# Kernel tuning notes

Hardware: AMD Instinct MI355X
Metric: run time of the kernel (lower is better)

## Reference

```python
import jax, jax.numpy as jnp
import numpy as np

NUM_HEADS = 16
D_ATT = 64


def setup_inputs() -> dict:
    key = jax.random.key(0)
    ks = jax.random.split(key, 7)
    b, n, hd = 4, 2048, NUM_HEADS * 64  # input last dim = num_heads * per-head embed_dim
    Q_vec = jax.random.normal(ks[0], (b, n, hd), dtype=jnp.float32)
    K_vec = jax.random.normal(ks[1], (b, n, hd), dtype=jnp.float32)
    V_vec = jax.random.normal(ks[2], (b, n, hd), dtype=jnp.float32)
    # torch Linear weights: [out_features, in_features] = [d_attention, per_head_dim]
    W_Q = jax.random.normal(ks[3], (D_ATT, 64), dtype=jnp.float32) * 0.02
    W_K = jax.random.normal(ks[4], (D_ATT, 64), dtype=jnp.float32) * 0.02
    W_V = jax.random.normal(ks[5], (D_ATT, 64), dtype=jnp.float32) * 0.02
    mask = jax.random.bernoulli(ks[6], p=0.9, shape=(b, n))  # bool [b, n]
    return {"Q_vec": Q_vec, "K_vec": K_vec, "V_vec": V_vec,
            "W_Q": W_Q, "W_K": W_K, "W_V": W_V, "mask": mask}


def reference(Q_vec, K_vec, V_vec, W_Q, W_K, W_V, mask):
    b, n, _ = Q_vec.shape
    h = NUM_HEADS
    scaling = 1.0 / np.sqrt(D_ATT).astype(np.float32)

    def split_heads(x):  # b n (h d) -> b h n d
        return x.reshape(b, n, h, -1).transpose(0, 2, 1, 3)

    # Linear applied per-head (weights are [out, in]; y = x @ W^T)
    q = split_heads(Q_vec) @ W_Q.T  # [b,h,n,D_ATT]
    k = split_heads(K_vec) @ W_K.T
    v = split_heads(V_vec) @ W_V.T

    dots = jnp.einsum('bhid,bhjd->bhij', q, k) * scaling  # [b,h,n,n]
    pair_mask = mask[:, None, :] & mask[:, :, None]       # [b,n,n]
    mask_value = -jnp.finfo(dots.dtype).max
    dots = jnp.where(pair_mask[:, None, :, :], dots, mask_value)
    attn = jax.nn.softmax(dots, axis=-1)
    out = jnp.einsum('bhij,bhjd->bhid', attn, v)          # [b,h,n,D_ATT]
    return out.transpose(0, 2, 1, 3).reshape(b, n, h * D_ATT)
```

## Files before the change

### kernel.cpp

```cpp
#include <hip/hip_runtime.h>

#define B_  4
#define N_  2048
#define H_  16
#define HD_ 1024

typedef short  bf16x8 __attribute__((ext_vector_type(8)));
typedef short  bf16x4 __attribute__((ext_vector_type(4)));
typedef float  f32x4  __attribute__((ext_vector_type(4)));

static __device__ __forceinline__ unsigned short f2bf(float f) {
    unsigned int u = __builtin_bit_cast(unsigned int, f);
    u += 0x7FFFu + ((u >> 16) & 1u);
    return (unsigned short)(u >> 16);
}

static __device__ __forceinline__ unsigned rne_hi(float f) {
    unsigned u = __builtin_bit_cast(unsigned, f);
    return u + 0x7FFFu + ((u >> 16) & 1u);
}
static __device__ __forceinline__ unsigned f2bf2pack(float lo, float hi) {
    return __builtin_amdgcn_perm(rne_hi(hi), rne_hi(lo), 0x07060302u);
}

__global__ __launch_bounds__(256) void proj_kernel(
    const float* __restrict__ Qv, const float* __restrict__ Kv,
    const float* __restrict__ Vv, const float* __restrict__ WQ,
    const float* __restrict__ WK, const float* __restrict__ WV,
    unsigned short* __restrict__ qs, unsigned short* __restrict__ ks,
    unsigned short* __restrict__ vt)
{
    __shared__ __align__(16) unsigned short xb[64][72];
    __shared__ __align__(16) unsigned short Wb[64][72];
    unsigned short (*sb)[72] = xb;

    const int tid  = threadIdx.x;
    const int wq   = tid >> 6;
    const int lane = tid & 63;
    const int l15  = lane & 15;
    const int quad = lane >> 4;

    const int i0 = blockIdx.x * 64;
    const int h  = blockIdx.y;
    const int bz = blockIdx.z;
    const int b  = bz / 3;
    const int p  = bz - b * 3;

    const size_t inbase = ((size_t)b * N_ + i0) * HD_ + h * 64;
    const size_t bh     = (size_t)b * H_ + h;

    const float* W   = (p == 0) ? WQ : (p == 1) ? WK : WV;
    const float* inp = ((p == 0) ? Qv : (p == 1) ? Kv : Vv) + inbase;

    for (int v = tid; v < 1024; v += 256) {
        int tok = v >> 4, c4 = (v & 15) * 4;
        float4 f = *reinterpret_cast<const float4*>(inp + (size_t)tok * HD_ + c4);
        uint2 u;
        u.x = f2bf2pack(f.x, f.y);
        u.y = f2bf2pack(f.z, f.w);
        *reinterpret_cast<uint2*>(&xb[tok][c4]) = u;
        float4 g = *reinterpret_cast<const float4*>(W + (size_t)v * 4);
        uint2 w2;
        w2.x = f2bf2pack(g.x, g.y);
        w2.y = f2bf2pack(g.z, g.w);
        *reinterpret_cast<uint2*>(&Wb[tok][c4]) = w2;
    }
    __syncthreads();

    bf16x8 ax[2];
    #pragma unroll
    for (int kh = 0; kh < 2; ++kh)
        ax[kh] = *reinterpret_cast<const bf16x8*>(&xb[wq * 16 + l15][kh * 32 + quad * 8]);

    f32x4 C[4];
    #pragma unroll
    for (int t = 0; t < 4; ++t) {
        C[t] = f32x4{0.f, 0.f, 0.f, 0.f};
        #pragma unroll
        for (int kh = 0; kh < 2; ++kh) {
            bf16x8 bw = *reinterpret_cast<const bf16x8*>(&Wb[t * 16 + l15][kh * 32 + quad * 8]);
            C[t] = __builtin_amdgcn_mfma_f32_16x16x32_bf16(ax[kh], bw, C[t], 0, 0, 0);
        }
    }

    __syncthreads();

    if (p < 2) {
        const float scl = (p == 0) ? 0.180336880f : 1.f;
        #pragma unroll
        for (int t = 0; t < 4; ++t)
            #pragma unroll
            for (int r = 0; r < 4; ++r)
                sb[wq * 16 + quad * 4 + r][t * 16 + l15] = f2bf(C[t][r] * scl);
        __syncthreads();
        unsigned short* dst = ((p == 0) ? qs : ks) + ((size_t)bh * N_ + i0) * 64;
        for (int v = tid; v < 512; v += 256) {
            int row = v >> 3, c0 = (v & 7) * 8;
            *reinterpret_cast<uint4*>(dst + (size_t)row * 64 + c0) =
                *reinterpret_cast<const uint4*>(&sb[row][c0]);
        }
    } else {
        #pragma unroll
        for (int t = 0; t < 4; ++t) {
            uint2 u;
            u.x = f2bf2pack(C[t][0], C[t][1]);
            u.y = f2bf2pack(C[t][2], C[t][3]);
            *reinterpret_cast<uint2*>(&sb[t * 16 + l15][wq * 16 + quad * 4]) = u;
        }
        __syncthreads();
        unsigned short* vdst = vt + (size_t)bh * 64 * N_ + i0;
        for (int v = tid; v < 512; v += 256) {
            int d = v >> 3, c0 = (v & 7) * 8;
            *reinterpret_cast<uint4*>(vdst + (size_t)d * N_ + c0) =
                *reinterpret_cast<const uint4*>(&sb[d][c0]);
        }
    }
}

__global__ __launch_bounds__(256, 2) void attn_kernel(
    const unsigned short* __restrict__ qs, const unsigned short* __restrict__ ks,
    const unsigned short* __restrict__ vt, const int* __restrict__ maskp,
    float* __restrict__ out)
{
    __shared__ __align__(16) unsigned short Ks[64][72];
    __shared__ __align__(16) unsigned short Vt[64][68];
    __shared__ float kb[64];

    const int tid  = threadIdx.x;
    const int w    = tid >> 6;
    const int lane = tid & 63;
    const int l15  = lane & 15;
    const int quad = lane >> 4;

    const int i0 = blockIdx.x * 256;
    const int bh = blockIdx.y;
    const int b  = bh >> 4;
    const int h  = bh & 15;
    const int qrow0 = i0 + w * 64;

    bf16x8 aq[4][2];
    float  qm[4];
    #pragma unroll
    for (int rt = 0; rt < 4; ++rt) {
        const unsigned short* qrow = qs + ((size_t)bh * N_ + qrow0 + rt * 16 + l15) * 64;
        aq[rt][0] = *reinterpret_cast<const bf16x8*>(qrow + quad * 8);
        aq[rt][1] = *reinterpret_cast<const bf16x8*>(qrow + 32 + quad * 8);
        qm[rt] = maskp[b * N_ + qrow0 + rt * 16 + l15] ? 1.f : 0.f;
    }

    bf16x8 aones;
    #pragma unroll
    for (int j = 0; j < 8; ++j) aones[j] = (short)0x3F80;

    f32x4 O[4][4];
    f32x4 L[4];
    #pragma unroll
    for (int rt = 0; rt < 4; ++rt) {
        L[rt] = f32x4{0.f, 0.f, 0.f, 0.f};
        #pragma unroll
        for (int c = 0; c < 4; ++c) O[rt][c] = f32x4{0.f, 0.f, 0.f, 0.f};
    }

    const unsigned short* kbase = ks + (size_t)bh * N_ * 64;
    const unsigned short* vbase = vt + (size_t)bh * 64 * N_;

    for (int kv0 = 0; kv0 < N_; kv0 += 64) {
        __syncthreads();
        #pragma unroll
        for (int it = 0; it < 2; ++it) {
            int idx = tid + it * 256;
            int r = idx >> 3, g = idx & 7;
            *reinterpret_cast<uint4*>(&Ks[r][g * 8]) =
                *reinterpret_cast<const uint4*>(kbase + (size_t)(kv0 + r) * 64 + g * 8);
        }
        #pragma unroll
        for (int it = 0; it < 4; ++it) {
            int idx = tid + it * 256;
            int r = idx >> 4, g2 = idx & 15;
            *reinterpret_cast<uint2*>(&Vt[r][g2 * 4]) =
                *reinterpret_cast<const uint2*>(vbase + (size_t)r * N_ + kv0 + g2 * 4);
        }
        if (tid < 64) kb[tid] = maskp[b * N_ + kv0 + tid] ? 0.f : -1e30f;
        __syncthreads();

        bf16x8 ak[4][2];
        #pragma unroll
        for (int ct = 0; ct < 4; ++ct)
            #pragma unroll
            for (int kh = 0; kh < 2; ++kh)
                ak[ct][kh] = *reinterpret_cast<const bf16x8*>(&Ks[ct * 16 + l15][kh * 32 + quad * 8]);

        bf16x8 av[4][2];
        #pragma unroll
        for (int ct = 0; ct < 4; ++ct)
            #pragma unroll
            for (int kh = 0; kh < 2; ++kh) {
                bf16x4 lo = *reinterpret_cast<const bf16x4*>(&Vt[ct * 16 + l15][kh * 32 + quad * 4]);
                bf16x4 hi = *reinterpret_cast<const bf16x4*>(&Vt[ct * 16 + l15][kh * 32 + 16 + quad * 4]);
                av[ct][kh] = bf16x8{lo[0], lo[1], lo[2], lo[3], hi[0], hi[1], hi[2], hi[3]};
            }

        f32x4 kbv[4];
        #pragma unroll
        for (int ct = 0; ct < 4; ++ct)
            kbv[ct] = *reinterpret_cast<const f32x4*>(&kb[ct * 16 + quad * 4]);

        #pragma unroll
        for (int rt = 0; rt < 4; ++rt) {
            f32x4 S[4];
            #pragma unroll
            for (int ct = 0; ct < 4; ++ct) {
                S[ct] = kbv[ct];
                #pragma unroll
                for (int kh = 0; kh < 2; ++kh)
                    S[ct] = __builtin_amdgcn_mfma_f32_16x16x32_bf16(ak[ct][kh], aq[rt][kh], S[ct], 0, 0, 0);
            }
            unsigned pk[4][2];
            #pragma unroll
            for (int ct = 0; ct < 4; ++ct) {
                float e0 = __builtin_amdgcn_exp2f(S[ct][0] * qm[rt]);
                float e1 = __builtin_amdgcn_exp2f(S[ct][1] * qm[rt]);
                float e2 = __builtin_amdgcn_exp2f(S[ct][2] * qm[rt]);
                float e3 = __builtin_amdgcn_exp2f(S[ct][3] * qm[rt]);
                pk[ct][0] = f2bf2pack(e0, e1);
                pk[ct][1] = f2bf2pack(e2, e3);
            }
            bf16x8 ap[2];
            #pragma unroll
            for (int kh = 0; kh < 2; ++kh) {
                uint4 u = uint4{pk[2 * kh][0], pk[2 * kh][1], pk[2 * kh + 1][0], pk[2 * kh + 1][1]};
                ap[kh] = __builtin_bit_cast(bf16x8, u);
            }
            #pragma unroll
            for (int kh = 0; kh < 2; ++kh)
                L[rt] = __builtin_amdgcn_mfma_f32_16x16x32_bf16(aones, ap[kh], L[rt], 0, 0, 0);
            #pragma unroll
            for (int ct = 0; ct < 4; ++ct)
                #pragma unroll
                for (int kh = 0; kh < 2; ++kh)
                    O[rt][ct] = __builtin_amdgcn_mfma_f32_16x16x32_bf16(av[ct][kh], ap[kh], O[rt][ct], 0, 0, 0);
        }
    }

    #pragma unroll
    for (int rt = 0; rt < 4; ++rt) {
        float inv = 1.f / L[rt][0];
        float* orow = out + ((size_t)b * N_ + qrow0 + rt * 16 + l15) * HD_ + h * 64 + quad * 4;
        #pragma unroll
        for (int ct = 0; ct < 4; ++ct)
            #pragma unroll
            for (int r = 0; r < 4; ++r)
                orow[ct * 16 + r] = O[rt][ct][r] * inv;
    }
}

extern "C" void kernel_launch(void* const* d_in, const int* in_sizes, int n_in,
                              void* d_out, int out_size, void* d_ws, size_t ws_size,
                              hipStream_t stream)
{
    const float* Qv  = (const float*)d_in[0];
    const float* Kv  = (const float*)d_in[1];
    const float* Vv  = (const float*)d_in[2];
    const float* WQ  = (const float*)d_in[3];
    const float* WK  = (const float*)d_in[4];
    const float* WV  = (const float*)d_in[5];
    const int*   msk = (const int*)d_in[6];
    float* out = (float*)d_out;

    const size_t per = (size_t)B_ * H_ * N_ * 64;
    unsigned short* qsb = (unsigned short*)d_ws;
    unsigned short* ksb = qsb + per;
    unsigned short* vtb = ksb + per;

    proj_kernel<<<dim3(N_ / 64, H_, B_ * 3), 256, 0, stream>>>(Qv, Kv, Vv, WQ, WK, WV, qsb, ksb, vtb);
    attn_kernel<<<dim3(N_ / 256, B_ * H_), 256, 0, stream>>>(qsb, ksb, vtb, msk, out);
}
```

Before: 238.2 us.

## Pre-convert projection weights to bf16 and load operands directly into registers

```diff
diff --git a/kernel.cpp b/kernel.cpp
--- a/kernel.cpp
+++ b/kernel.cpp
@@ -11,28 +11,47 @@
 
 static __device__ __forceinline__ unsigned short f2bf(float f) {
     unsigned int u = __builtin_bit_cast(unsigned int, f);
-    u += 0x7FFFu + ((u >> 16) & 1u);
-    return (unsigned short)(u >> 16);
-}
-
-static __device__ __forceinline__ unsigned rne_hi(float f) {
-    unsigned u = __builtin_bit_cast(unsigned, f);
-    return u + 0x7FFFu + ((u >> 16) & 1u);
+    return (unsigned short)((u + 0x8000u) >> 16);
 }
 static __device__ __forceinline__ unsigned f2bf2pack(float lo, float hi) {
-    return __builtin_amdgcn_perm(rne_hi(hi), rne_hi(lo), 0x07060302u);
+    unsigned a = __builtin_bit_cast(unsigned, lo) + 0x8000u;
+    unsigned b = __builtin_bit_cast(unsigned, hi) + 0x8000u;
+    return __builtin_amdgcn_perm(b, a, 0x07060302u);
+}
+
+__global__ __launch_bounds__(256) void wconv_kernel(
+    const float* __restrict__ WQ, const float* __restrict__ WK,
+    const float* __restrict__ WV, unsigned short* __restrict__ wbf)
+{
+    const int p = blockIdx.x;
+    const float* W = (p == 0) ? WQ : (p == 1) ? WK : WV;
+    const float scl = (p == 0) ? 0.180336880f : 1.f;
+    const int t = threadIdx.x;
+    const float* src = W + t * 16;
+    unsigned short* dst = wbf + p * 4096 + t * 16;
+    float4 f[4];
+    #pragma unroll
+    for (int i = 0; i < 4; ++i) f[i] = *reinterpret_cast<const float4*>(src + i * 4);
+    uint4 o0, o1;
+    o0.x = f2bf2pack(f[0].x * scl, f[0].y * scl);
+    o0.y = f2bf2pack(f[0].z * scl, f[0].w * scl);
+    o0.z = f2bf2pack(f[1].x * scl, f[1].y * scl);
+    o0.w = f2bf2pack(f[1].z * scl, f[1].w * scl);
+    o1.x = f2bf2pack(f[2].x * scl, f[2].y * scl);
+    o1.y = f2bf2pack(f[2].z * scl, f[2].w * scl);
+    o1.z = f2bf2pack(f[3].x * scl, f[3].y * scl);
+    o1.w = f2bf2pack(f[3].z * scl, f[3].w * scl);
+    *reinterpret_cast<uint4*>(dst)     = o0;
+    *reinterpret_cast<uint4*>(dst + 8) = o1;
 }
 
 __global__ __launch_bounds__(256) void proj_kernel(
     const float* __restrict__ Qv, const float* __restrict__ Kv,
-    const float* __restrict__ Vv, const float* __restrict__ WQ,
-    const float* __restrict__ WK, const float* __restrict__ WV,
+    const float* __restrict__ Vv, const unsigned short* __restrict__ wbf,
     unsigned short* __restrict__ qs, unsigned short* __restrict__ ks,
     unsigned short* __restrict__ vt)
 {
-    __shared__ __align__(16) unsigned short xb[64][72];
-    __shared__ __align__(16) unsigned short Wb[64][72];
-    unsigned short (*sb)[72] = xb;
+    __shared__ __align__(16) unsigned short sb[64][72];
 
     const int tid  = threadIdx.x;
     const int wq   = tid >> 6;
@@ -46,56 +65,50 @@
     const int b  = bz / 3;
     const int p  = bz - b * 3;
 
-    const size_t inbase = ((size_t)b * N_ + i0) * HD_ + h * 64;
-    const size_t bh     = (size_t)b * H_ + h;
-
-    const float* W   = (p == 0) ? WQ : (p == 1) ? WK : WV;
-    const float* inp = ((p == 0) ? Qv : (p == 1) ? Kv : Vv) + inbase;
-
-    for (int v = tid; v < 1024; v += 256) {
-        int tok = v >> 4, c4 = (v & 15) * 4;
-        float4 f = *reinterpret_cast<const float4*>(inp + (size_t)tok * HD_ + c4);
-        uint2 u;
-        u.x = f2bf2pack(f.x, f.y);
-        u.y = f2bf2pack(f.z, f.w);
-        *reinterpret_cast<uint2*>(&xb[tok][c4]) = u;
-        float4 g = *reinterpret_cast<const float4*>(W + (size_t)v * 4);
-        uint2 w2;
-        w2.x = f2bf2pack(g.x, g.y);
-        w2.y = f2bf2pack(g.z, g.w);
-        *reinterpret_cast<uint2*>(&Wb[tok][c4]) = w2;
-    }
-    __syncthreads();
-
+    const size_t bh = (size_t)b * H_ + h;
+    const float* inp = ((p == 0) ? Qv : (p == 1) ? Kv : Vv)
+                       + ((size_t)b * N_ + i0) * HD_ + h * 64;
+
+    const unsigned short* wb = wbf + p * 4096;
+    bf16x8 bw[4][2];
+    #pragma unroll
+    for (int t = 0; t < 4; ++t)
+        #pragma unroll
+        for (int kh = 0; kh < 2; ++kh)
+            bw[t][kh] = *reinterpret_cast<const bf16x8*>(wb + (t * 16 + l15) * 64 + kh * 32 + quad * 8);
+
+    const float* xp = inp + (size_t)(wq * 16 + l15) * HD_;
     bf16x8 ax[2];
     #pragma unroll
-    for (int kh = 0; kh < 2; ++kh)
-        ax[kh] = *reinterpret_cast<const bf16x8*>(&xb[wq * 16 + l15][kh * 32 + quad * 8]);
+    for (int kh = 0; kh < 2; ++kh) {
+        float4 f0 = *reinterpret_cast<const float4*>(xp + kh * 32 + quad * 8);
+        float4 f1 = *reinterpret_cast<const float4*>(xp + kh * 32 + quad * 8 + 4);
+        uint4 u = uint4{f2bf2pack(f0.x, f0.y), f2bf2pack(f0.z, f0.w),
+                        f2bf2pack(f1.x, f1.y), f2bf2pack(f1.z, f1.w)};
+        ax[kh] = __builtin_bit_cast(bf16x8, u);
+    }
 
     f32x4 C[4];
     #pragma unroll
     for (int t = 0; t < 4; ++t) {
         C[t] = f32x4{0.f, 0.f, 0.f, 0.f};
         #pragma unroll
-        for (int kh = 0; kh < 2; ++kh) {
-            bf16x8 bw = *reinterpret_cast<const bf16x8*>(&Wb[t * 16 + l15][kh * 32 + quad * 8]);
-            C[t] = __builtin_amdgcn_mfma_f32_16x16x32_bf16(ax[kh], bw, C[t], 0, 0, 0);
-        }
-    }
-
-    __syncthreads();
+        for (int kh = 0; kh < 2; ++kh)
+            C[t] = __builtin_amdgcn_mfma_f32_16x16x32_bf16(ax[kh], bw[t][kh], C[t], 0, 0, 0);
+    }
 
     if (p < 2) {
-        const float scl = (p == 0) ? 0.180336880f : 1.f;
         #pragma unroll
         for (int t = 0; t < 4; ++t)
             #pragma unroll
             for (int r = 0; r < 4; ++r)
-                sb[wq * 16 + quad * 4 + r][t * 16 + l15] = f2bf(C[t][r] * scl);
+                sb[wq * 16 + quad * 4 + r][t * 16 + l15] = f2bf(C[t][r]);
         __syncthreads();
         unsigned short* dst = ((p == 0) ? qs : ks) + ((size_t)bh * N_ + i0) * 64;
-        for (int v = tid; v < 512; v += 256) {
-            int row = v >> 3, c0 = (v & 7) * 8;
+        #pragma unroll
+        for (int v = 0; v < 2; ++v) {
+            int idx = tid + v * 256;
+            int row = idx >> 3, c0 = (idx & 7) * 8;
             *reinterpret_cast<uint4*>(dst + (size_t)row * 64 + c0) =
                 *reinterpret_cast<const uint4*>(&sb[row][c0]);
         }
@@ -109,8 +122,10 @@
         }
         __syncthreads();
         unsigned short* vdst = vt + (size_t)bh * 64 * N_ + i0;
-        for (int v = tid; v < 512; v += 256) {
-            int d = v >> 3, c0 = (v & 7) * 8;
+        #pragma unroll
+        for (int v = 0; v < 2; ++v) {
+            int idx = tid + v * 256;
+            int d = idx >> 3, c0 = (idx & 7) * 8;
             *reinterpret_cast<uint4*>(vdst + (size_t)d * N_ + c0) =
                 *reinterpret_cast<const uint4*>(&sb[d][c0]);
         }
@@ -271,7 +286,9 @@
     unsigned short* qsb = (unsigned short*)d_ws;
     unsigned short* ksb = qsb + per;
     unsigned short* vtb = ksb + per;
-
-    proj_kernel<<<dim3(N_ / 64, H_, B_ * 3), 256, 0, stream>>>(Qv, Kv, Vv, WQ, WK, WV, qsb, ksb, vtb);
+    unsigned short* wbf = vtb + per;
+
+    wconv_kernel<<<dim3(3), 256, 0, stream>>>(WQ, WK, WV, wbf);
+    proj_kernel<<<dim3(N_ / 64, H_, B_ * 3), 256, 0, stream>>>(Qv, Kv, Vv, wbf, qsb, ksb, vtb);
     attn_kernel<<<dim3(N_ / 256, B_ * H_), 256, 0, stream>>>(qsb, ksb, vtb, msk, out);
 }
```

Measured after the change: 238.1 us. Within noise of the previous version (-0.0%).

## Pre-swizzle V into MFMA fragment layout and load it directly from global

Applied to the files above, without the earlier changes.

```diff
diff --git a/kernel.cpp b/kernel.cpp
--- a/kernel.cpp
+++ b/kernel.cpp
@@ -11,16 +11,12 @@
 
 static __device__ __forceinline__ unsigned short f2bf(float f) {
     unsigned int u = __builtin_bit_cast(unsigned int, f);
-    u += 0x7FFFu + ((u >> 16) & 1u);
-    return (unsigned short)(u >> 16);
-}
-
-static __device__ __forceinline__ unsigned rne_hi(float f) {
-    unsigned u = __builtin_bit_cast(unsigned, f);
-    return u + 0x7FFFu + ((u >> 16) & 1u);
+    return (unsigned short)((u + 0x8000u) >> 16);
 }
 static __device__ __forceinline__ unsigned f2bf2pack(float lo, float hi) {
-    return __builtin_amdgcn_perm(rne_hi(hi), rne_hi(lo), 0x07060302u);
+    unsigned a = __builtin_bit_cast(unsigned, lo) + 0x8000u;
+    unsigned b = __builtin_bit_cast(unsigned, hi) + 0x8000u;
+    return __builtin_amdgcn_perm(b, a, 0x07060302u);
 }
 
 __global__ __launch_bounds__(256) void proj_kernel(
@@ -83,9 +79,8 @@
         }
     }
 
-    __syncthreads();
-
     if (p < 2) {
+        __syncthreads();
         const float scl = (p == 0) ? 0.180336880f : 1.f;
         #pragma unroll
         for (int t = 0; t < 4; ++t)
@@ -100,19 +95,14 @@
                 *reinterpret_cast<const uint4*>(&sb[row][c0]);
         }
     } else {
+        unsigned short* vf = vt + (size_t)bh * 64 * N_ + (size_t)blockIdx.x * 4096;
         #pragma unroll
         for (int t = 0; t < 4; ++t) {
             uint2 u;
             u.x = f2bf2pack(C[t][0], C[t][1]);
             u.y = f2bf2pack(C[t][2], C[t][3]);
-            *reinterpret_cast<uint2*>(&sb[t * 16 + l15][wq * 16 + quad * 4]) = u;
-        }
-        __syncthreads();
-        unsigned short* vdst = vt + (size_t)bh * 64 * N_ + i0;
-        for (int v = tid; v < 512; v += 256) {
-            int d = v >> 3, c0 = (v & 7) * 8;
-            *reinterpret_cast<uint4*>(vdst + (size_t)d * N_ + c0) =
-                *reinterpret_cast<const uint4*>(&sb[d][c0]);
+            *reinterpret_cast<uint2*>(vf + ((t * 2 + (wq >> 1)) * 16 + l15) * 32
+                                         + quad * 8 + (wq & 1) * 4) = u;
         }
     }
 }
@@ -123,7 +113,6 @@
     float* __restrict__ out)
 {
     __shared__ __align__(16) unsigned short Ks[64][72];
-    __shared__ __align__(16) unsigned short Vt[64][68];
     __shared__ float kb[64];
 
     const int tid  = threadIdx.x;
@@ -132,8 +121,12 @@
     const int l15  = lane & 15;
     const int quad = lane >> 4;
 
-    const int i0 = blockIdx.x * 256;
-    const int bh = blockIdx.y;
+    const int lin  = blockIdx.y * gridDim.x + blockIdx.x;
+    const int xcd  = lin & 7;
+    const int bh   = xcd * 8 + (lin >> 6);
+    const int xblk = (lin >> 3) & 7;
+
+    const int i0 = xblk * 256;
     const int b  = bh >> 4;
     const int h  = bh & 15;
     const int qrow0 = i0 + w * 64;
@@ -162,7 +155,7 @@
     }
 
     const unsigned short* kbase = ks + (size_t)bh * N_ * 64;
-    const unsigned short* vbase = vt + (size_t)bh * 64 * N_;
+    const unsigned short* vfb   = vt + (size_t)bh * 64 * N_;
 
     for (int kv0 = 0; kv0 < N_; kv0 += 64) {
         __syncthreads();
@@ -173,13 +166,6 @@
             *reinterpret_cast<uint4*>(&Ks[r][g * 8]) =
                 *reinterpret_cast<const uint4*>(kbase + (size_t)(kv0 + r) * 64 + g * 8);
         }
-        #pragma unroll
-        for (int it = 0; it < 4; ++it) {
-            int idx = tid + it * 256;
-            int r = idx >> 4, g2 = idx & 15;
-            *reinterpret_cast<uint2*>(&Vt[r][g2 * 4]) =
-                *reinterpret_cast<const uint2*>(vbase + (size_t)r * N_ + kv0 + g2 * 4);
-        }
         if (tid < 64) kb[tid] = maskp[b * N_ + kv0 + tid] ? 0.f : -1e30f;
         __syncthreads();
 
@@ -190,15 +176,14 @@
             for (int kh = 0; kh < 2; ++kh)
                 ak[ct][kh] = *reinterpret_cast<const bf16x8*>(&Ks[ct * 16 + l15][kh * 32 + quad * 8]);
 
+        const unsigned short* vf = vfb + (size_t)(kv0 >> 6) * 4096;
         bf16x8 av[4][2];
         #pragma unroll
         for (int ct = 0; ct < 4; ++ct)
             #pragma unroll
-            for (int kh = 0; kh < 2; ++kh) {
-                bf16x4 lo = *reinterpret_cast<const bf16x4*>(&Vt[ct * 16 + l15][kh * 32 + quad * 4]);
-                bf16x4 hi = *reinterpret_cast<const bf16x4*>(&Vt[ct * 16 + l15][kh * 32 + 16 + quad * 4]);
-                av[ct][kh] = bf16x8{lo[0], lo[1], lo[2], lo[3], hi[0], hi[1], hi[2], hi[3]};
-            }
+            for (int kh = 0; kh < 2; ++kh)
+                av[ct][kh] = *reinterpret_cast<const bf16x8*>(
+                    vf + ((ct * 2 + kh) * 16 + l15) * 32 + quad * 8);
 
         f32x4 kbv[4];
         #pragma unroll
```

Measured after the change: 227.9 us. 4.3% less time.
